# Kernel optimization log

Hardware: AMD Instinct MI355X
Metric: run time of the kernel (lower is better)

The kernel has to match this reference:

```python
import jax, jax.numpy as jnp
import numpy as np

N_NODES = 100000
N_EDGES = 1000000
DIM_IN = 64
DIM_H = 64
DIM_OUT = 1


def _lin_init(key, out_dim, in_dim):
    # torch Linear default: U(-1/sqrt(fan_in), 1/sqrt(fan_in))
    bound = 1.0 / np.sqrt(in_dim)
    return jax.random.uniform(key, (out_dim, in_dim), jnp.float32, -bound, bound)


def setup_inputs() -> dict:
    key = jax.random.key(0)
    ks = jax.random.split(key, 10)
    x = jax.random.normal(ks[0], (N_NODES, DIM_IN), jnp.float32)
    edge_index = jax.random.randint(ks[1], (2, N_EDGES), 0, N_NODES, dtype=jnp.int64)
    # layer 0: SAGEConv(DIM_IN, DIM_H): lin_l (with bias) on aggregated neighbors, lin_r (no bias) on root
    Wl0 = _lin_init(ks[2], DIM_H, DIM_IN)
    bl0 = jax.random.uniform(ks[3], (DIM_H,), jnp.float32, -1.0 / np.sqrt(DIM_IN), 1.0 / np.sqrt(DIM_IN))
    Wr0 = _lin_init(ks[4], DIM_H, DIM_IN)
    # layer 1: SAGEConv(DIM_H, DIM_OUT)
    Wl1 = _lin_init(ks[5], DIM_OUT, DIM_H)
    bl1 = jax.random.uniform(ks[6], (DIM_OUT,), jnp.float32, -1.0 / np.sqrt(DIM_H), 1.0 / np.sqrt(DIM_H))
    Wr1 = _lin_init(ks[7], DIM_OUT, DIM_H)
    return {"x": x, "edge_index": edge_index,
            "Wl0": Wl0, "bl0": bl0, "Wr0": Wr0,
            "Wl1": Wl1, "bl1": bl1, "Wr1": Wr1}


def sage_conv(h, src, dst, Wl, bl, Wr):
    # messages: gather source-node features per edge, mean-aggregate into destination nodes
    msg = h[src]                                                   # [E, d]
    summed = jax.ops.segment_sum(msg, dst, num_segments=N_NODES)   # [N, d]
    deg = jax.ops.segment_sum(jnp.ones((src.shape[0],), h.dtype), dst, num_segments=N_NODES)
    mean_nb = summed / jnp.maximum(deg, 1.0)[:, None]
    # out = lin_l(mean_neighbors) + lin_r(x_root)
    return mean_nb @ Wl.T + bl + h @ Wr.T


def reference(x, edge_index, Wl0, bl0, Wr0, Wl1, bl1, Wr1):
    src, dst = edge_index[0], edge_index[1]
    h = sage_conv(x, src, dst, Wl0, bl0, Wr0)
    h = jax.nn.relu(h)  # dropout is identity in eval mode
    h = sage_conv(h, src, dst, Wl1, bl1, Wr1)
    return (h, jax.nn.sigmoid(h))
```

## Files before the change

### kernel.cpp

```cpp
#include <hip/hip_runtime.h>
#include <hip/hip_bf16.h>
#include <math.h>

#define N_NODES 100000
#define N_EDGES 1000000
#define DIM 64
#define SCAN_BLOCKS 391
#define AGPAD 72
#define NHB 125
#define HTHREADS 1024
#define EPB (N_EDGES / NHB)
#define HWORDS ((N_NODES + 3) / 4)
#define HALF_NODES (N_NODES / 2)
#define HWORDS_HALF (HALF_NODES / 4)

typedef __hip_bfloat16 bf16;
typedef __attribute__((ext_vector_type(8))) short short8;
typedef __attribute__((ext_vector_type(4))) float floatx4;

__device__ __forceinline__ float b2f(bf16 v) { return __bfloat162float(v); }

__device__ __forceinline__ unsigned int packbf2(float a, float b) {
    bf16 x = __float2bfloat16(a), y = __float2bfloat16(b);
    unsigned short ux = *(unsigned short*)&x, uy = *(unsigned short*)&y;
    return (unsigned int)ux | ((unsigned int)uy << 16);
}

__device__ __forceinline__ short f2bs(float v) {
    bf16 x = __float2bfloat16(v);
    return *(short*)&x;
}

__device__ __forceinline__ float2 upk(unsigned int u) {
    unsigned short lo = (unsigned short)(u & 0xffff);
    unsigned short hi = (unsigned short)(u >> 16);
    bf16 a = *(bf16*)&lo, b = *(bf16*)&hi;
    return make_float2(b2f(a), b2f(b));
}

__device__ __forceinline__ int clampN(int v) {
    return v < 0 ? 0 : (v >= N_NODES ? N_NODES - 1 : v);
}


__global__ __launch_bounds__(HTHREADS) void count_kernel(const int* __restrict__ ei,
                                                         unsigned int* __restrict__ bh32) {
    __shared__ unsigned int cnt[HWORDS_HALF];
    const int t = threadIdx.x;
    const int seg = blockIdx.x >> 1, half = blockIdx.x & 1;
    const int nlo = half * HALF_NODES, nhi = nlo + HALF_NODES;
    for (int w = t; w < HWORDS_HALF; w += HTHREADS) cnt[w] = 0u;
    __syncthreads();
    const int4* dst4 = (const int4*)(ei + N_EDGES + seg * EPB);
    for (int k = t; k < EPB / 4; k += HTHREADS) {
        int4 d4 = dst4[k];
        int d;
        d = clampN(d4.x); if (d >= nlo && d < nhi) { int ld = d - nlo; atomicAdd(&cnt[ld >> 2], 1u << (8 * (ld & 3))); }
        d = clampN(d4.y); if (d >= nlo && d < nhi) { int ld = d - nlo; atomicAdd(&cnt[ld >> 2], 1u << (8 * (ld & 3))); }
        d = clampN(d4.z); if (d >= nlo && d < nhi) { int ld = d - nlo; atomicAdd(&cnt[ld >> 2], 1u << (8 * (ld & 3))); }
        d = clampN(d4.w); if (d >= nlo && d < nhi) { int ld = d - nlo; atomicAdd(&cnt[ld >> 2], 1u << (8 * (ld & 3))); }
    }
    __syncthreads();
    unsigned int* out = bh32 + (long)seg * HWORDS + half * HWORDS_HALF;
    for (int w = t; w < HWORDS_HALF; w += HTHREADS) out[w] = cnt[w];
}

__global__ void scan1_convert_kernel(unsigned char* __restrict__ bhb,
                                     int* __restrict__ degi,
                                     int* __restrict__ rowstart,
                                     int* __restrict__ bsum,
                                     const float4* __restrict__ x4,
                                     uint2* __restrict__ xb4,
                                     const float* __restrict__ Wl0,
                                     const float* __restrict__ Wr0,
                                     short* __restrict__ wt) {
    __shared__ int sc[256];
    int b = blockIdx.x;
    int t = threadIdx.x;
    if (b >= SCAN_BLOCKS) {
        int bb = b - SCAN_BLOCKS;
        if (bb < 6250) {
            int idx = bb * 256 + t;
            float4 f = x4[idx];
            xb4[idx] = make_uint2(packbf2(f.x, f.y), packbf2(f.z, f.w));
        } else {
            for (int i = t; i < 8192; i += 256) {
                int d = i >> 7, k = i & 127;
                float v = (k < 64) ? Wl0[d * 64 + k] : Wr0[d * 64 + (k - 64)];
                wt[i] = f2bs(v);
            }
        }
        return;
    }
    int i = b * 256 + t;
    int v = 0;
    if (i < N_NODES) {
        int sum = 0;
        #pragma unroll 5
        for (int c = 0; c < NHB; ++c) {
            long off = (long)c * (HWORDS * 4) + i;
            int u = bhb[off];
            bhb[off] = (unsigned char)sum;
            sum += u;
        }
        degi[i] = sum;
        v = sum;
    }
    sc[t] = v;
    __syncthreads();
    #pragma unroll
    for (int off = 1; off < 256; off <<= 1) {
        int u = (t >= off) ? sc[t - off] : 0;
        __syncthreads();
        sc[t] += u;
        __syncthreads();
    }
    if (i < N_NODES) rowstart[i] = sc[t] - v;
    if (t == 255) bsum[b] = sc[t];
}

__global__ void scan2_kernel(int* __restrict__ bsum) {
    __shared__ int sc[512];
    int t = threadIdx.x;
    int v = (t < SCAN_BLOCKS) ? bsum[t] : 0;
    sc[t] = v;
    __syncthreads();
    #pragma unroll
    for (int off = 1; off < 512; off <<= 1) {
        int u = (t >= off) ? sc[t - off] : 0;
        __syncthreads();
        sc[t] += u;
        __syncthreads();
    }
    if (t < SCAN_BLOCKS) bsum[t] = sc[t] - v;
}

__global__ __launch_bounds__(HTHREADS) void fill_kernel(const int* __restrict__ ei,
                                                        const int* __restrict__ rowstart,
                                                        const int* __restrict__ bsum,
                                                        const unsigned int* __restrict__ bh32,
                                                        int* __restrict__ csr) {
    __shared__ unsigned int cnt[HWORDS_HALF];
    const int t = threadIdx.x;
    const int seg = blockIdx.x >> 1, half = blockIdx.x & 1;
    const int nlo = half * HALF_NODES, nhi = nlo + HALF_NODES;
    const unsigned int* in = bh32 + (long)seg * HWORDS + half * HWORDS_HALF;
    for (int w = t; w < HWORDS_HALF; w += HTHREADS) cnt[w] = in[w];
    __syncthreads();
    const int4* srcp4 = (const int4*)(ei + seg * EPB);
    const int4* dstp4 = (const int4*)(ei + N_EDGES + seg * EPB);
    for (int k = t; k < EPB / 4; k += HTHREADS) {
        int4 s4 = srcp4[k];
        int4 d4 = dstp4[k];
        int d, ld, sv;
        unsigned int old;
        d = clampN(d4.x);
        if (d >= nlo && d < nhi) {
            ld = d - nlo; sv = clampN(s4.x);
            old = atomicAdd(&cnt[ld >> 2], 1u << (8 * (ld & 3)));
            csr[rowstart[d] + bsum[d >> 8] + (int)((old >> (8 * (ld & 3))) & 0xffu)] = sv;
        }
        d = clampN(d4.y);
        if (d >= nlo && d < nhi) {
            ld = d - nlo; sv = clampN(s4.y);
            old = atomicAdd(&cnt[ld >> 2], 1u << (8 * (ld & 3)));
            csr[rowstart[d] + bsum[d >> 8] + (int)((old >> (8 * (ld & 3))) & 0xffu)] = sv;
        }
        d = clampN(d4.z);
        if (d >= nlo && d < nhi) {
            ld = d - nlo; sv = clampN(s4.z);
            old = atomicAdd(&cnt[ld >> 2], 1u << (8 * (ld & 3)));
            csr[rowstart[d] + bsum[d >> 8] + (int)((old >> (8 * (ld & 3))) & 0xffu)] = sv;
        }
        d = clampN(d4.w);
        if (d >= nlo && d < nhi) {
            ld = d - nlo; sv = clampN(s4.w);
            old = atomicAdd(&cnt[ld >> 2], 1u << (8 * (ld & 3)));
            csr[rowstart[d] + bsum[d >> 8] + (int)((old >> (8 * (ld & 3))) & 0xffu)] = sv;
        }
    }
}

__global__ __launch_bounds__(256) void agg_gemm_kernel(
        const uint2* __restrict__ xb2, const short* __restrict__ xb,
        const short* __restrict__ wt,
        const int* __restrict__ rowstart, const int* __restrict__ bsum,
        const int* __restrict__ degi, const int* __restrict__ csr,
        const float* __restrict__ bl0, const float* __restrict__ Wl1,
        const float* __restrict__ Wr1,
        float* __restrict__ s, float* __restrict__ t) {
    __shared__ short As[16 * AGPAD];
    __shared__ float sRed[16], tRed[16];
    const int tid = threadIdx.x;
    const int nb = blockIdx.x * 16;

    if (tid < 16) { sRed[tid] = 0.0f; tRed[tid] = 0.0f; }

    {
        int qn = tid >> 4;
        int l  = tid & 15;
        int n = nb + qn;
        int beg = rowstart[n] + bsum[n >> 8];
        int cnt = degi[n];
        float4 A0 = make_float4(0.f, 0.f, 0.f, 0.f);
        float4 A1 = A0, A2 = A0, A3 = A0;
        int i = 0;
        if (cnt >= 8) {
            const int* cp = csr + beg;
            int e0 = cp[0], e1 = cp[1], e2 = cp[2], e3 = cp[3];
            int e4 = cp[4], e5 = cp[5], e6 = cp[6], e7 = cp[7];
            for (;;) {
                uint2 u0 = xb2[(long)e0 * 16 + l];
                uint2 u1 = xb2[(long)e1 * 16 + l];
                uint2 u2 = xb2[(long)e2 * 16 + l];
                uint2 u3 = xb2[(long)e3 * 16 + l];
                uint2 u4 = xb2[(long)e4 * 16 + l];
                uint2 u5 = xb2[(long)e5 * 16 + l];
                uint2 u6 = xb2[(long)e6 * 16 + l];
                uint2 u7 = xb2[(long)e7 * 16 + l];
                int ni = i + 8;
                bool more = (ni + 8 <= cnt);
                int f0, f1, f2, f3, f4, f5, f6, f7;
                if (more) {
                    const int* np = csr + beg + ni;
                    f0 = np[0]; f1 = np[1]; f2 = np[2]; f3 = np[3];
                    f4 = np[4]; f5 = np[5]; f6 = np[6]; f7 = np[7];
                }
                float2 f;
                f = upk(u0.x); A0.x += f.x; A0.y += f.y; f = upk(u0.y); A0.z += f.x; A0.w += f.y;
                f = upk(u1.x); A1.x += f.x; A1.y += f.y; f = upk(u1.y); A1.z += f.x; A1.w += f.y;
                f = upk(u2.x); A2.x += f.x; A2.y += f.y; f = upk(u2.y); A2.z += f.x; A2.w += f.y;
                f = upk(u3.x); A3.x += f.x; A3.y += f.y; f = upk(u3.y); A3.z += f.x; A3.w += f.y;
                f = upk(u4.x); A0.x += f.x; A0.y += f.y; f = upk(u4.y); A0.z += f.x; A0.w += f.y;
                f = upk(u5.x); A1.x += f.x; A1.y += f.y; f = upk(u5.y); A1.z += f.x; A1.w += f.y;
                f = upk(u6.x); A2.x += f.x; A2.y += f.y; f = upk(u6.y); A2.z += f.x; A2.w += f.y;
                f = upk(u7.x); A3.x += f.x; A3.y += f.y; f = upk(u7.y); A3.z += f.x; A3.w += f.y;
                i = ni;
                if (!more) break;
                e0 = f0; e1 = f1; e2 = f2; e3 = f3;
                e4 = f4; e5 = f5; e6 = f6; e7 = f7;
            }
        }
        if (i + 4 <= cnt) {
            int e0 = csr[beg + i],     e1 = csr[beg + i + 1];
            int e2 = csr[beg + i + 2], e3 = csr[beg + i + 3];
            uint2 u0 = xb2[(long)e0 * 16 + l];
            uint2 u1 = xb2[(long)e1 * 16 + l];
            uint2 u2 = xb2[(long)e2 * 16 + l];
            uint2 u3 = xb2[(long)e3 * 16 + l];
            float2 f;
            f = upk(u0.x); A0.x += f.x; A0.y += f.y; f = upk(u0.y); A0.z += f.x; A0.w += f.y;
            f = upk(u1.x); A1.x += f.x; A1.y += f.y; f = upk(u1.y); A1.z += f.x; A1.w += f.y;
            f = upk(u2.x); A2.x += f.x; A2.y += f.y; f = upk(u2.y); A2.z += f.x; A2.w += f.y;
            f = upk(u3.x); A3.x += f.x; A3.y += f.y; f = upk(u3.y); A3.z += f.x; A3.w += f.y;
            i += 4;
        }
        if (i < cnt) {
            uint2 u = xb2[(long)csr[beg + i] * 16 + l];
            float2 f = upk(u.x); A0.x += f.x; A0.y += f.y;
            f = upk(u.y); A0.z += f.x; A0.w += f.y;
        }
        if (i + 1 < cnt) {
            uint2 u = xb2[(long)csr[beg + i + 1] * 16 + l];
            float2 f = upk(u.x); A1.x += f.x; A1.y += f.y;
            f = upk(u.y); A1.z += f.x; A1.w += f.y;
        }
        if (i + 2 < cnt) {
            uint2 u = xb2[(long)csr[beg + i + 2] * 16 + l];
            float2 f = upk(u.x); A2.x += f.x; A2.y += f.y;
            f = upk(u.y); A2.z += f.x; A2.w += f.y;
        }
        float inv = 1.0f / fmaxf((float)cnt, 1.0f);
        float ax = (A0.x + A1.x + A2.x + A3.x) * inv;
        float ay = (A0.y + A1.y + A2.y + A3.y) * inv;
        float az = (A0.z + A1.z + A2.z + A3.z) * inv;
        float aw = (A0.w + A1.w + A2.w + A3.w) * inv;
        *(uint2*)&As[qn * AGPAD + 4 * l] =
            make_uint2(packbf2(ax, ay), packbf2(az, aw));
    }
    __syncthreads();

    const int lane = tid & 63;
    const int w = tid >> 6;
    const int r = lane & 15;
    const int quad = lane >> 4;

    short8 a0 = *(const short8*)&As[r * AGPAD + quad * 8];
    short8 a1 = *(const short8*)&As[r * AGPAD + 32 + quad * 8];
    const long xrow = (long)(nb + r) * 64 + quad * 8;
    short8 a2 = *(const short8*)(xb + xrow);
    short8 a3 = *(const short8*)(xb + xrow + 32);

    const int d = w * 16 + r;
    const short* brow = wt + (long)d * 128 + quad * 8;
    short8 b0 = *(const short8*)(brow);
    short8 b1 = *(const short8*)(brow + 32);
    short8 b2 = *(const short8*)(brow + 64);
    short8 b3 = *(const short8*)(brow + 96);

    float bb = bl0[d];
    floatx4 acc = {bb, bb, bb, bb};
    acc = __builtin_amdgcn_mfma_f32_16x16x32_bf16(a0, b0, acc, 0, 0, 0);
    acc = __builtin_amdgcn_mfma_f32_16x16x32_bf16(a1, b1, acc, 0, 0, 0);
    acc = __builtin_amdgcn_mfma_f32_16x16x32_bf16(a2, b2, acc, 0, 0, 0);
    acc = __builtin_amdgcn_mfma_f32_16x16x32_bf16(a3, b3, acc, 0, 0, 0);

    float w1 = Wl1[d], w2 = Wr1[d];
    float hs[4], ht[4];
    #pragma unroll
    for (int g = 0; g < 4; ++g) {
        float h = fmaxf(acc[g], 0.0f);
        hs[g] = h * w1;
        ht[g] = h * w2;
    }
    #pragma unroll
    for (int g = 0; g < 4; ++g) {
        #pragma unroll
        for (int off = 1; off < 16; off <<= 1) {
            hs[g] += __shfl_xor(hs[g], off, 64);
            ht[g] += __shfl_xor(ht[g], off, 64);
        }
    }
    if (r == 0) {
        #pragma unroll
        for (int g = 0; g < 4; ++g) {
            atomicAdd(&sRed[quad * 4 + g], hs[g]);
            atomicAdd(&tRed[quad * 4 + g], ht[g]);
        }
    }
    __syncthreads();
    if (tid < 16) {
        s[nb + tid] = sRed[tid];
        t[nb + tid] = tRed[tid];
    }
}

__global__ void final_kernel(const float* __restrict__ s,
                             const float* __restrict__ t,
                             const int* __restrict__ rowstart,
                             const int* __restrict__ bsum,
                             const int* __restrict__ degi,
                             const int* __restrict__ csr,
                             const float* __restrict__ bl1,
                             float* __restrict__ out) {
    int n = blockIdx.x * 256 + threadIdx.x;
    if (n >= N_NODES) return;
    int beg = rowstart[n] + bsum[n >> 8];
    int cnt = degi[n];
    float acc = 0.0f;
    int i = 0;
    for (; i + 4 <= cnt; i += 4) {
        int e0 = csr[beg + i], e1 = csr[beg + i + 1];
        int e2 = csr[beg + i + 2], e3 = csr[beg + i + 3];
        acc += s[e0] + s[e1] + s[e2] + s[e3];
    }
    for (; i < cnt; ++i) acc += s[csr[beg + i]];
    float v = acc / fmaxf((float)cnt, 1.0f) + bl1[0] + t[n];
    float sg = 1.0f / (1.0f + expf(-v));
    out[n] = v;
    out[N_NODES + n] = sg;
}

extern "C" void kernel_launch(void* const* d_in, const int* in_sizes, int n_in,
                              void* d_out, int out_size, void* d_ws, size_t ws_size,
                              hipStream_t stream) {
    const float* x   = (const float*)d_in[0];
    const int*   ei  = (const int*)d_in[1];
    const float* Wl0 = (const float*)d_in[2];
    const float* bl0 = (const float*)d_in[3];
    const float* Wr0 = (const float*)d_in[4];
    const float* Wl1 = (const float*)d_in[5];
    const float* bl1 = (const float*)d_in[6];
    const float* Wr1 = (const float*)d_in[7];
    float* out = (float*)d_out;

    char* ws = (char*)d_ws;
    int*   degi     = (int*)(ws);
    int*   rowstart = (int*)(ws + 400000);
    int*   bsum     = (int*)(ws + 800000);
    float* s        = (float*)(ws + 804096);
    float* t        = (float*)(ws + 1204096);
    int*   csr      = (int*)(ws + 1604096);
    char*  xb       = (ws + 5604096);
    short* wt       = (short*)(ws + 18404096);
    char*  bh       = (ws + 18420480);

    count_kernel<<<2 * NHB, HTHREADS, 0, stream>>>(ei, (unsigned int*)bh);
    scan1_convert_kernel<<<SCAN_BLOCKS + 6251, 256, 0, stream>>>(
        (unsigned char*)bh, degi, rowstart, bsum,
        (const float4*)x, (uint2*)xb, Wl0, Wr0, wt);
    scan2_kernel<<<1, 512, 0, stream>>>(bsum);
    fill_kernel<<<2 * NHB, HTHREADS, 0, stream>>>(ei, rowstart, bsum,
                                                  (const unsigned int*)bh, csr);
    agg_gemm_kernel<<<6250, 256, 0, stream>>>((const uint2*)xb, (const short*)xb,
                                              wt, rowstart, bsum, degi, csr,
                                              bl0, Wl1, Wr1, s, t);
    final_kernel<<<SCAN_BLOCKS, 256, 0, stream>>>(s, t, rowstart, bsum, degi, csr,
                                                  bl1, out);
}
```

Before: 170.9 us.

## Fuse CSR build stages into one cooperative kernel with grid syncs

```diff
diff --git a/kernel.cpp b/kernel.cpp
--- a/kernel.cpp
+++ b/kernel.cpp
@@ -1,14 +1,18 @@
 #include <hip/hip_runtime.h>
+#include <hip/hip_cooperative_groups.h>
 #include <hip/hip_bf16.h>
 #include <math.h>
+
+namespace cg = cooperative_groups;
 
 #define N_NODES 100000
 #define N_EDGES 1000000
 #define DIM 64
-#define SCAN_BLOCKS 391
+#define NCHUNK 391
 #define AGPAD 72
 #define NHB 125
-#define HTHREADS 1024
+#define BTHREADS 1024
+#define BBLOCKS (2 * NHB)
 #define EPB (N_EDGES / NHB)
 #define HWORDS ((N_NODES + 3) / 4)
 #define HALF_NODES (N_NODES / 2)
@@ -42,146 +46,154 @@
     return v < 0 ? 0 : (v >= N_NODES ? N_NODES - 1 : v);
 }
 
-
-__global__ __launch_bounds__(HTHREADS) void count_kernel(const int* __restrict__ ei,
-                                                         unsigned int* __restrict__ bh32) {
+__global__ __launch_bounds__(BTHREADS) void build_kernel(
+        const int* __restrict__ ei,
+        unsigned int* __restrict__ bh32,
+        const float4* __restrict__ x4,
+        uint2* __restrict__ xb4,
+        const float* __restrict__ Wl0,
+        const float* __restrict__ Wr0,
+        short* __restrict__ wt,
+        int* __restrict__ degi,
+        int* __restrict__ rowstart,
+        int* __restrict__ chsum,
+        int* __restrict__ bsum,
+        int* __restrict__ csr) {
     __shared__ unsigned int cnt[HWORDS_HALF];
-    const int t = threadIdx.x;
-    const int seg = blockIdx.x >> 1, half = blockIdx.x & 1;
+    __shared__ int sc[512];
+    __shared__ int bsumL[NCHUNK];
+    cg::grid_group grid = cg::this_grid();
+
+    const int t = threadIdx.x, b = blockIdx.x;
+    const int seg = b >> 1, half = b & 1;
     const int nlo = half * HALF_NODES, nhi = nlo + HALF_NODES;
-    for (int w = t; w < HWORDS_HALF; w += HTHREADS) cnt[w] = 0u;
+
+    for (int w = t; w < HWORDS_HALF; w += BTHREADS) cnt[w] = 0u;
     __syncthreads();
-    const int4* dst4 = (const int4*)(ei + N_EDGES + seg * EPB);
-    for (int k = t; k < EPB / 4; k += HTHREADS) {
-        int4 d4 = dst4[k];
-        int d;
-        d = clampN(d4.x); if (d >= nlo && d < nhi) { int ld = d - nlo; atomicAdd(&cnt[ld >> 2], 1u << (8 * (ld & 3))); }
-        d = clampN(d4.y); if (d >= nlo && d < nhi) { int ld = d - nlo; atomicAdd(&cnt[ld >> 2], 1u << (8 * (ld & 3))); }
-        d = clampN(d4.z); if (d >= nlo && d < nhi) { int ld = d - nlo; atomicAdd(&cnt[ld >> 2], 1u << (8 * (ld & 3))); }
-        d = clampN(d4.w); if (d >= nlo && d < nhi) { int ld = d - nlo; atomicAdd(&cnt[ld >> 2], 1u << (8 * (ld & 3))); }
-    }
-    __syncthreads();
-    unsigned int* out = bh32 + (long)seg * HWORDS + half * HWORDS_HALF;
-    for (int w = t; w < HWORDS_HALF; w += HTHREADS) out[w] = cnt[w];
-}
-
-__global__ void scan1_convert_kernel(unsigned char* __restrict__ bhb,
-                                     int* __restrict__ degi,
-                                     int* __restrict__ rowstart,
-                                     int* __restrict__ bsum,
-                                     const float4* __restrict__ x4,
-                                     uint2* __restrict__ xb4,
-                                     const float* __restrict__ Wl0,
-                                     const float* __restrict__ Wr0,
-                                     short* __restrict__ wt) {
-    __shared__ int sc[256];
-    int b = blockIdx.x;
-    int t = threadIdx.x;
-    if (b >= SCAN_BLOCKS) {
-        int bb = b - SCAN_BLOCKS;
-        if (bb < 6250) {
-            int idx = bb * 256 + t;
+    {
+        const int4* dst4 = (const int4*)(ei + N_EDGES + seg * EPB);
+        for (int k = t; k < EPB / 4; k += BTHREADS) {
+            int4 d4 = dst4[k];
+            int d;
+            d = clampN(d4.x); if (d >= nlo && d < nhi) { int ld = d - nlo; atomicAdd(&cnt[ld >> 2], 1u << (8 * (ld & 3))); }
+            d = clampN(d4.y); if (d >= nlo && d < nhi) { int ld = d - nlo; atomicAdd(&cnt[ld >> 2], 1u << (8 * (ld & 3))); }
+            d = clampN(d4.z); if (d >= nlo && d < nhi) { int ld = d - nlo; atomicAdd(&cnt[ld >> 2], 1u << (8 * (ld & 3))); }
+            d = clampN(d4.w); if (d >= nlo && d < nhi) { int ld = d - nlo; atomicAdd(&cnt[ld >> 2], 1u << (8 * (ld & 3))); }
+        }
+        __syncthreads();
+        unsigned int* outp = bh32 + (long)seg * HWORDS + half * HWORDS_HALF;
+        for (int w = t; w < HWORDS_HALF; w += BTHREADS) outp[w] = cnt[w];
+        const int cbase = b * 6400;
+        for (int j = t; j < 6400; j += BTHREADS) {
+            int idx = cbase + j;
             float4 f = x4[idx];
             xb4[idx] = make_uint2(packbf2(f.x, f.y), packbf2(f.z, f.w));
-        } else {
-            for (int i = t; i < 8192; i += 256) {
+        }
+        if (b == 0) {
+            for (int i = t; i < 8192; i += BTHREADS) {
                 int d = i >> 7, k = i & 127;
                 float v = (k < 64) ? Wl0[d * 64 + k] : Wr0[d * 64 + (k - 64)];
                 wt[i] = f2bs(v);
             }
         }
-        return;
-    }
-    int i = b * 256 + t;
-    int v = 0;
-    if (i < N_NODES) {
-        int sum = 0;
-        #pragma unroll 5
-        for (int c = 0; c < NHB; ++c) {
-            long off = (long)c * (HWORDS * 4) + i;
-            int u = bhb[off];
-            bhb[off] = (unsigned char)sum;
-            sum += u;
-        }
-        degi[i] = sum;
-        v = sum;
-    }
-    sc[t] = v;
-    __syncthreads();
-    #pragma unroll
-    for (int off = 1; off < 256; off <<= 1) {
-        int u = (t >= off) ? sc[t - off] : 0;
+    }
+    grid.sync();
+
+    {
+        unsigned char* bhb = (unsigned char*)bh32;
+        for (int chunk = b; chunk < NCHUNK; chunk += BBLOCKS) {
+            int i = chunk * 256 + t;
+            int v = 0;
+            if (t < 256 && i < N_NODES) {
+                int sum = 0;
+                #pragma unroll 5
+                for (int c = 0; c < NHB; ++c) {
+                    long off = (long)c * (HWORDS * 4) + i;
+                    int u = bhb[off];
+                    bhb[off] = (unsigned char)sum;
+                    sum += u;
+                }
+                degi[i] = sum;
+                v = sum;
+            }
+            if (t < 256) sc[t] = v;
+            __syncthreads();
+            #pragma unroll
+            for (int off = 1; off < 256; off <<= 1) {
+                int u = 0;
+                if (t < 256 && t >= off) u = sc[t - off];
+                __syncthreads();
+                if (t < 256) sc[t] += u;
+                __syncthreads();
+            }
+            if (t < 256 && i < N_NODES) rowstart[i] = sc[t] - v;
+            if (t == 255) chsum[chunk] = sc[255];
+            __syncthreads();
+        }
+    }
+    grid.sync();
+
+    {
+        int v = 0;
+        if (t < 512) {
+            v = (t < NCHUNK) ? chsum[t] : 0;
+            sc[t] = v;
+        }
         __syncthreads();
-        sc[t] += u;
+        #pragma unroll
+        for (int off = 1; off < 512; off <<= 1) {
+            int u = 0;
+            if (t < 512 && t >= off) u = sc[t - off];
+            __syncthreads();
+            if (t < 512) sc[t] += u;
+            __syncthreads();
+        }
+        if (t < NCHUNK) {
+            bsumL[t] = sc[t] - v;
+            if (b == 0) bsum[t] = sc[t] - v;
+        }
+    }
+
+    {
+        const unsigned int* inp = bh32 + (long)seg * HWORDS + half * HWORDS_HALF;
+        for (int w = t; w < HWORDS_HALF; w += BTHREADS) cnt[w] = inp[w];
         __syncthreads();
-    }
-    if (i < N_NODES) rowstart[i] = sc[t] - v;
-    if (t == 255) bsum[b] = sc[t];
-}
-
-__global__ void scan2_kernel(int* __restrict__ bsum) {
-    __shared__ int sc[512];
-    int t = threadIdx.x;
-    int v = (t < SCAN_BLOCKS) ? bsum[t] : 0;
-    sc[t] = v;
-    __syncthreads();
-    #pragma unroll
-    for (int off = 1; off < 512; off <<= 1) {
-        int u = (t >= off) ? sc[t - off] : 0;
-        __syncthreads();
-        sc[t] += u;
-        __syncthreads();
-    }
-    if (t < SCAN_BLOCKS) bsum[t] = sc[t] - v;
-}
-
-__global__ __launch_bounds__(HTHREADS) void fill_kernel(const int* __restrict__ ei,
-                                                        const int* __restrict__ rowstart,
-                                                        const int* __restrict__ bsum,
-                                                        const unsigned int* __restrict__ bh32,
-                                                        int* __restrict__ csr) {
-    __shared__ unsigned int cnt[HWORDS_HALF];
-    const int t = threadIdx.x;
-    const int seg = blockIdx.x >> 1, half = blockIdx.x & 1;
-    const int nlo = half * HALF_NODES, nhi = nlo + HALF_NODES;
-    const unsigned int* in = bh32 + (long)seg * HWORDS + half * HWORDS_HALF;
-    for (int w = t; w < HWORDS_HALF; w += HTHREADS) cnt[w] = in[w];
-    __syncthreads();
-    const int4* srcp4 = (const int4*)(ei + seg * EPB);
-    const int4* dstp4 = (const int4*)(ei + N_EDGES + seg * EPB);
-    for (int k = t; k < EPB / 4; k += HTHREADS) {
-        int4 s4 = srcp4[k];
-        int4 d4 = dstp4[k];
-        int d, ld, sv;
-        unsigned int old;
-        d = clampN(d4.x);
-        if (d >= nlo && d < nhi) {
-            ld = d - nlo; sv = clampN(s4.x);
-            old = atomicAdd(&cnt[ld >> 2], 1u << (8 * (ld & 3)));
-            csr[rowstart[d] + bsum[d >> 8] + (int)((old >> (8 * (ld & 3))) & 0xffu)] = sv;
-        }
-        d = clampN(d4.y);
-        if (d >= nlo && d < nhi) {
-            ld = d - nlo; sv = clampN(s4.y);
-            old = atomicAdd(&cnt[ld >> 2], 1u << (8 * (ld & 3)));
-            csr[rowstart[d] + bsum[d >> 8] + (int)((old >> (8 * (ld & 3))) & 0xffu)] = sv;
-        }
-        d = clampN(d4.z);
-        if (d >= nlo && d < nhi) {
-            ld = d - nlo; sv = clampN(s4.z);
-            old = atomicAdd(&cnt[ld >> 2], 1u << (8 * (ld & 3)));
-            csr[rowstart[d] + bsum[d >> 8] + (int)((old >> (8 * (ld & 3))) & 0xffu)] = sv;
-        }
-        d = clampN(d4.w);
-        if (d >= nlo && d < nhi) {
-            ld = d - nlo; sv = clampN(s4.w);
-            old = atomicAdd(&cnt[ld >> 2], 1u << (8 * (ld & 3)));
-            csr[rowstart[d] + bsum[d >> 8] + (int)((old >> (8 * (ld & 3))) & 0xffu)] = sv;
-        }
-    }
-}
-
-__global__ __launch_bounds__(256) void agg_gemm_kernel(
+        const int4* srcp4 = (const int4*)(ei + seg * EPB);
+        const int4* dstp4 = (const int4*)(ei + N_EDGES + seg * EPB);
+        for (int k = t; k < EPB / 4; k += BTHREADS) {
+            int4 s4 = srcp4[k];
+            int4 d4 = dstp4[k];
+            int d, ld, sv;
+            unsigned int old;
+            d = clampN(d4.x);
+            if (d >= nlo && d < nhi) {
+                ld = d - nlo; sv = clampN(s4.x);
+                old = atomicAdd(&cnt[ld >> 2], 1u << (8 * (ld & 3)));
+                csr[rowstart[d] + bsumL[d >> 8] + (int)((old >> (8 * (ld & 3))) & 0xffu)] = sv;
+            }
+            d = clampN(d4.y);
+            if (d >= nlo && d < nhi) {
+                ld = d - nlo; sv = clampN(s4.y);
+                old = atomicAdd(&cnt[ld >> 2], 1u << (8 * (ld & 3)));
+                csr[rowstart[d] + bsumL[d >> 8] + (int)((old >> (8 * (ld & 3))) & 0xffu)] = sv;
+            }
+            d = clampN(d4.z);
+            if (d >= nlo && d < nhi) {
+                ld = d - nlo; sv = clampN(s4.z);
+                old = atomicAdd(&cnt[ld >> 2], 1u << (8 * (ld & 3)));
+                csr[rowstart[d] + bsumL[d >> 8] + (int)((old >> (8 * (ld & 3))) & 0xffu)] = sv;
+            }
+            d = clampN(d4.w);
+            if (d >= nlo && d < nhi) {
+                ld = d - nlo; sv = clampN(s4.w);
+                old = atomicAdd(&cnt[ld >> 2], 1u << (8 * (ld & 3)));
+                csr[rowstart[d] + bsumL[d >> 8] + (int)((old >> (8 * (ld & 3))) & 0xffu)] = sv;
+            }
+        }
+    }
+}
+
+__global__ __launch_bounds__(256, 8) void agg_gemm_kernel(
         const uint2* __restrict__ xb2, const short* __restrict__ xb,
         const short* __restrict__ wt,
         const int* __restrict__ rowstart, const int* __restrict__ bsum,
@@ -349,6 +361,15 @@
     int cnt = degi[n];
     float acc = 0.0f;
     int i = 0;
+    for (; i + 8 <= cnt; i += 8) {
+        int e0 = csr[beg + i],     e1 = csr[beg + i + 1];
+        int e2 = csr[beg + i + 2], e3 = csr[beg + i + 3];
+        int e4 = csr[beg + i + 4], e5 = csr[beg + i + 5];
+        int e6 = csr[beg + i + 6], e7 = csr[beg + i + 7];
+        float v0 = s[e0], v1 = s[e1], v2 = s[e2], v3 = s[e3];
+        float v4 = s[e4], v5 = s[e5], v6 = s[e6], v7 = s[e7];
+        acc += ((v0 + v1) + (v2 + v3)) + ((v4 + v5) + (v6 + v7));
+    }
     for (; i + 4 <= cnt; i += 4) {
         int e0 = csr[beg + i], e1 = csr[beg + i + 1];
         int e2 = csr[beg + i + 2], e3 = csr[beg + i + 3];
@@ -378,6 +399,7 @@
     int*   degi     = (int*)(ws);
     int*   rowstart = (int*)(ws + 400000);
     int*   bsum     = (int*)(ws + 800000);
+    int*   chsum    = (int*)(ws + 802048);
     float* s        = (float*)(ws + 804096);
     float* t        = (float*)(ws + 1204096);
     int*   csr      = (int*)(ws + 1604096);
@@ -385,16 +407,18 @@
     short* wt       = (short*)(ws + 18404096);
     char*  bh       = (ws + 18420480);
 
-    count_kernel<<<2 * NHB, HTHREADS, 0, stream>>>(ei, (unsigned int*)bh);
-    scan1_convert_kernel<<<SCAN_BLOCKS + 6251, 256, 0, stream>>>(
-        (unsigned char*)bh, degi, rowstart, bsum,
-        (const float4*)x, (uint2*)xb, Wl0, Wr0, wt);
-    scan2_kernel<<<1, 512, 0, stream>>>(bsum);
-    fill_kernel<<<2 * NHB, HTHREADS, 0, stream>>>(ei, rowstart, bsum,
-                                                  (const unsigned int*)bh, csr);
+    unsigned int* bh32 = (unsigned int*)bh;
+    const float4* x4 = (const float4*)x;
+    uint2* xb4 = (uint2*)xb;
+    void* args[] = { (void*)&ei, (void*)&bh32, (void*)&x4, (void*)&xb4,
+                     (void*)&Wl0, (void*)&Wr0, (void*)&wt, (void*)&degi,
+                     (void*)&rowstart, (void*)&chsum, (void*)&bsum, (void*)&csr };
+    (void)hipLaunchCooperativeKernel((const void*)build_kernel,
+                                     dim3(BBLOCKS), dim3(BTHREADS),
+                                     args, 0, stream);
     agg_gemm_kernel<<<6250, 256, 0, stream>>>((const uint2*)xb, (const short*)xb,
                                               wt, rowstart, bsum, degi, csr,
                                               bl0, Wl1, Wr1, s, t);
-    final_kernel<<<SCAN_BLOCKS, 256, 0, stream>>>(s, t, rowstart, bsum, degi, csr,
-                                                  bl1, out);
-}
+    final_kernel<<<NCHUNK, 256, 0, stream>>>(s, t, rowstart, bsum, degi, csr,
+                                             bl1, out);
+}
```

Result: slower. 259.6 us (+51.9%).
